# Kernel tuning notes

Hardware: AMD Instinct MI355X
Metric: run time of the kernel (lower is better)

The kernel has to match this reference:

```python
import jax, jax.numpy as jnp
import numpy as np

EPS = 1e-5
DEG = 2  # polynomial degree of each resgconv layer (adj powers 0..DEG-1)


def _bn(x):
    # repo's functional batchnorm(x, axis=1): standardize over the node axis per event
    m = x.mean(axis=1, keepdims=True)
    s = x.std(axis=1, keepdims=True)
    return (x - m) / (s + EPS)


def _adj(phi, eta):
    # Gaussian kernel of squared euclidean distance in the (eta, phi) plane
    d2 = (phi[:, :, None] - phi[:, None, :]) ** 2 + (eta[:, :, None] - eta[:, None, :]) ** 2
    return jnp.exp(-d2)  # [B, N, N]


def _resgconv(adj, x, W, b, Wr, br):
    # x: [B, C_in, N]; spread = concat of adj^k @ x for k in 0..DEG-1 over channels
    sp = [x]
    cur = x
    for _ in range(DEG - 1):
        cur = jnp.einsum('bij,bcj->bci', adj, cur)
        sp.append(cur)
    sp = jnp.concatenate(sp, axis=1)  # [B, C_in*DEG, N]
    out = jnp.einsum('oc,bcn->bon', W, sp) + b[None, :, None]
    res = jnp.einsum('oc,bcn->bon', Wr, x) + br[None, :, None]  # residual shortcut
    return jax.nn.relu(out) + res


def setup_inputs():
    key = jax.random.key(0)
    ks = jax.random.split(key, 32)
    B, N = 16, 2048
    dims = [3, 64, 64, 64, 64]
    inp = {
        'e': jax.random.normal(ks[0], (B, N), dtype=jnp.float32),
        'phi': jax.random.normal(ks[1], (B, N), dtype=jnp.float32),
        'eta': jax.random.normal(ks[2], (B, N), dtype=jnp.float32),
    }
    for i in range(4):
        cin, cout = dims[i], dims[i + 1]
        inp[f'W{i}'] = jax.random.normal(ks[3 + 4 * i], (cout, cin * DEG)) * (1.0 / np.sqrt(cin * DEG))
        inp[f'b{i}'] = jnp.zeros((cout,), dtype=jnp.float32)
        inp[f'Wr{i}'] = jax.random.normal(ks[4 + 4 * i], (cout, cin)) * (1.0 / np.sqrt(cin))
        inp[f'br{i}'] = jnp.zeros((cout,), dtype=jnp.float32)
    inp['fcW'] = jax.random.normal(ks[30], (1, dims[-1])) * (1.0 / np.sqrt(dims[-1]))
    inp['fcb'] = jnp.zeros((1,), dtype=jnp.float32)
    return inp


def reference(e, phi, eta, W0, b0, Wr0, br0, W1, b1, Wr1, br1, W2, b2, Wr2, br2, W3, b3, Wr3, br3, fcW, fcb):
    en = _bn(e)
    adj = _adj(phi, eta)
    x = jnp.stack([en, _bn(eta), _bn(phi)], axis=1)  # [B, 3, N]
    for (W, b, Wr, br) in ((W0, b0, Wr0, br0), (W1, b1, Wr1, br1), (W2, b2, Wr2, br2), (W3, b3, Wr3, br3)):
        x = _resgconv(adj, x, W, b, Wr, br)
    pooled = x.mean(axis=2)  # [B, C]
    out = pooled @ fcW.T + fcb  # [B, 1]
    return out[:, 0]
```

## Files before the change

### kernel.cpp

```cpp
#include <hip/hip_runtime.h>
#include <hip/hip_bf16.h>

#define NN 2048
#define NB 16
#define CAT_PITCH 136
#define XT_OFF 16384
#define SMEM_BYTES 81920

typedef __attribute__((ext_vector_type(8))) short short8;
typedef __attribute__((ext_vector_type(4))) float f32x4;

static __device__ __forceinline__ float bfbits2f(short s) {
  unsigned int u = ((unsigned int)(unsigned short)s) << 16;
  float f; __builtin_memcpy(&f, &u, 4); return f;
}
static __device__ __forceinline__ short f2bfbits(float f) {
  __hip_bfloat16 h = __float2bfloat16(f);
  unsigned short us; __builtin_memcpy(&us, &h, 2); return (short)us;
}
static __device__ __forceinline__ float exp2_fast(float x) {
#if __has_builtin(__builtin_amdgcn_exp2f)
  return __builtin_amdgcn_exp2f(x);
#else
  return exp2f(x);
#endif
}
static __device__ __forceinline__ unsigned pack2bf(float f0, float f1) {
  unsigned u0, u1;
  __builtin_memcpy(&u0, &f0, 4);
  __builtin_memcpy(&u1, &f1, 4);
  return __builtin_amdgcn_perm(u1 + 0x8000u, u0 + 0x8000u, 0x07060302u);
}
static __device__ __forceinline__ void gload_lds16(const void* g, void* l) {
  __builtin_amdgcn_global_load_lds(
      (const __attribute__((address_space(1))) unsigned int*)g,
      (__attribute__((address_space(3))) unsigned int*)l, 16, 0, 0);
}

__global__ __launch_bounds__(256) void bnprep_kernel(
    const float* __restrict__ e, const float* __restrict__ phi,
    const float* __restrict__ eta, __hip_bfloat16* __restrict__ x0,
    const float* __restrict__ W0, const float* __restrict__ W1,
    const float* __restrict__ W2, const float* __restrict__ W3,
    const float* __restrict__ R0, const float* __restrict__ R1,
    const float* __restrict__ R2, const float* __restrict__ R3,
    short* __restrict__ blob) {
  const int t = threadIdx.x;
  if (blockIdx.y == 64) {
    const int layer = blockIdx.x;
    if (layer >= 4) return;
    const float* W = layer == 0 ? W0 : layer == 1 ? W1 : layer == 2 ? W2 : W3;
    const float* R = layer == 0 ? R0 : layer == 1 ? R1 : layer == 2 ? R2 : R3;
    const int CIN = layer == 0 ? 3 : 64;
    short* base = blob + layer * 24576;
    for (int f = t; f < 8192; f += 256) {
      int e8 = f & 7, ln = (f >> 3) & 63, ks = (f >> 9) & 3, os = f >> 11;
      int o = os * 16 + (ln & 15);
      int k = ks * 32 + (ln >> 4) * 8 + e8;
      float v = 0.f;
      if (k < 64) { if (k < CIN) v = W[o * 2 * CIN + k]; }
      else { int c = k - 64; if (c < CIN) v = W[o * 2 * CIN + CIN + c]; }
      short hi = f2bfbits(v);
      base[f] = hi;
      base[8192 + f] = f2bfbits(v - bfbits2f(hi));
    }
    for (int f = t; f < 4096; f += 256) {
      int e8 = f & 7, ln = (f >> 3) & 63, ks = (f >> 9) & 1, os = f >> 10;
      int o = os * 16 + (ln & 15);
      int k = ks * 32 + (ln >> 4) * 8 + e8;
      float v = (k < CIN) ? R[o * CIN + k] : 0.f;
      short hi = f2bfbits(v);
      base[16384 + f] = hi;
      base[20480 + f] = f2bfbits(v - bfbits2f(hi));
    }
    return;
  }
  const int b = blockIdx.x;
  const int c = blockIdx.y;
  __hip_bfloat16* out = x0 + ((size_t)b * 64 + c) * NN;
  if (c >= 3) {
    short8 z = {0, 0, 0, 0, 0, 0, 0, 0};
    for (int idx = t * 8; idx < NN; idx += 256 * 8) *(short8*)&out[idx] = z;
    return;
  }
  const float* src = (c == 0 ? e : (c == 1 ? eta : phi)) + (size_t)b * NN;
  float sum = 0.f, sq = 0.f;
  for (int idx = t * 4; idx < NN; idx += 256 * 4) {
    float4 v = *(const float4*)&src[idx];
    sum += v.x + v.y + v.z + v.w;
    sq += v.x * v.x + v.y * v.y + v.z * v.z + v.w * v.w;
  }
  __shared__ float rs[256], rq[256];
  rs[t] = sum; rq[t] = sq;
  __syncthreads();
  for (int off = 128; off > 0; off >>= 1) {
    if (t < off) { rs[t] += rs[t + off]; rq[t] += rq[t + off]; }
    __syncthreads();
  }
  const float m = rs[0] * (1.f / NN);
  const float var = fmaxf(rq[0] * (1.f / NN) - m * m, 0.f);
  const float rinv = 1.f / (sqrtf(var) + 1e-5f);
  for (int idx = t * 4; idx < NN; idx += 256 * 4) {
    float4 v = *(const float4*)&src[idx];
    out[idx + 0] = __float2bfloat16((v.x - m) * rinv);
    out[idx + 1] = __float2bfloat16((v.y - m) * rinv);
    out[idx + 2] = __float2bfloat16((v.z - m) * rinv);
    out[idx + 3] = __float2bfloat16((v.w - m) * rinv);
  }
}

__global__ __launch_bounds__(512, 4) void layer_kernel(
    const float* __restrict__ phi, const float* __restrict__ eta,
    const __hip_bfloat16* __restrict__ x, const short* __restrict__ wcat,
    const short* __restrict__ wrb, const float* __restrict__ bias,
    const float* __restrict__ brs, __hip_bfloat16* __restrict__ xo) {
  const int bid = blockIdx.x;
  const int sid = (bid & 7) * 64 + (bid >> 3);
  const int b = sid >> 5;
  const int i0 = (sid & 31) * 64;
  const int tid = threadIdx.x;
  const int wave = tid >> 6;
  const int lane = tid & 63;
  const int c0 = lane & 15;
  const int hh = lane >> 4;
  const int koff = hh * 8;
  const int rh = wave & 1;
  const int jg = wave >> 1;

  __shared__ __align__(16) char smem[SMEM_BYTES];
  float* phs = (float*)smem;
  float* ehs = phs + NN;

  const float SC = 1.20112240872f;
  {
    const float* pb = phi + (size_t)b * NN;
    const float* eb = eta + (size_t)b * NN;
    for (int idx = tid; idx < NN; idx += 512) {
      phs[idx] = pb[idx] * SC;
      ehs[idx] = eb[idx] * SC;
    }
  }
  const short* xb = (const short*)(x + (size_t)b * 64 * NN);

  const int d4 = lane & 1, d5 = (lane >> 1) & 1, d6 = (lane >> 2) & 1;
  const int d7 = (lane >> 3) & 1, d8 = (lane >> 4) & 1, d9 = (lane >> 5) & 1;
  const int ch_l = (d9 << 3) | (d8 << 2) | (d7 << 1) | (d6 ^ d8);
  const int jb8 = ((d5 ^ d7) << 1) | (d4 ^ d6 ^ d8);
  char* wbuf = smem + XT_OFF + wave * 8192;

#define STAGE(tt)                                                             \
  {                                                                           \
    const int _t = (tt);                                                      \
    _Pragma("unroll")                                                         \
    for (int gsl = 0; gsl < 4; ++gsl)                                         \
      gload_lds16(xb + (size_t)(gsl * 16 + ch_l) * NN + jg * 512 + _t * 32 +  \
                      jb8 * 8,                                                \
                  wbuf + (_t & 1) * 4096 + gsl * 1024);                       \
  }

  STAGE(0);
  __syncthreads();

  float pi_[2], ei_[2];
#pragma unroll
  for (int mt = 0; mt < 2; ++mt) {
    const int row = i0 + rh * 32 + mt * 16 + c0;
    pi_[mt] = phs[row];
    ei_[mt] = ehs[row];
  }

  f32x4 acc[2][4];
#pragma unroll
  for (int mt = 0; mt < 2; ++mt)
#pragma unroll
    for (int cs = 0; cs < 4; ++cs) acc[mt][cs] = (f32x4){0.f, 0.f, 0.f, 0.f};

#define COMPUTE(tt)                                                           \
  {                                                                           \
    const int _t = (tt);                                                      \
    const char* xbuf = wbuf + (_t & 1) * 4096;                                \
    const int jb = jg * 512 + _t * 32 + koff;                                 \
    float pj[8], ej[8];                                                       \
    *(float4*)&pj[0] = *(const float4*)&phs[jb];                              \
    *(float4*)&pj[4] = *(const float4*)&phs[jb + 4];                          \
    *(float4*)&ej[0] = *(const float4*)&ehs[jb];                              \
    *(float4*)&ej[4] = *(const float4*)&ehs[jb + 4];                          \
    short8 af[2];                                                             \
    _Pragma("unroll")                                                         \
    for (int mt = 0; mt < 2; ++mt) {                                          \
      unsigned au[4];                                                         \
      _Pragma("unroll")                                                       \
      for (int pp = 0; pp < 4; ++pp) {                                        \
        float dpa = pi_[mt] - pj[2 * pp],     dea = ei_[mt] - ej[2 * pp];     \
        float dpb = pi_[mt] - pj[2 * pp + 1], deb = ei_[mt] - ej[2 * pp + 1]; \
        float fa = exp2_fast(-(dpa * dpa + dea * dea));                       \
        float fb = exp2_fast(-(dpb * dpb + deb * deb));                       \
        au[pp] = pack2bf(fa, fb);                                             \
      }                                                                       \
      __builtin_memcpy(&af[mt], au, 16);                                      \
    }                                                                         \
    _Pragma("unroll")                                                         \
    for (int cs = 0; cs < 4; ++cs) {                                          \
      short8 bf = *(const short8*)(xbuf + cs * 1024 +                         \
                                   ((c0 * 64 + koff * 2) ^ ((c0 & 7) << 4))); \
      _Pragma("unroll")                                                       \
      for (int mt = 0; mt < 2; ++mt)                                          \
        acc[mt][cs] = __builtin_amdgcn_mfma_f32_16x16x32_bf16(af[mt], bf,     \
                                                          acc[mt][cs], 0, 0, 0); \
    }                                                                         \
  }

#pragma unroll 1
  for (int t = 0; t < 15; ++t) {
    STAGE(t + 1);
    __builtin_amdgcn_sched_barrier(0);
    asm volatile("s_waitcnt vmcnt(4)" ::: "memory");
    __builtin_amdgcn_sched_barrier(0);
    COMPUTE(t);
    __builtin_amdgcn_sched_barrier(0);
  }
  asm volatile("s_waitcnt vmcnt(0)" ::: "memory");
  __builtin_amdgcn_sched_barrier(0);
  COMPUTE(15);
  __syncthreads();

  char* xt = smem + XT_OFF;
  if (jg >= 2) {
    float* sp = (float*)(xt + (rh * 2 + (jg - 2)) * 8192);
#pragma unroll
    for (int mt = 0; mt < 2; ++mt)
#pragma unroll
      for (int cs = 0; cs < 4; ++cs)
        *(f32x4*)&sp[((mt * 4 + cs) * 64 + lane) * 4] = acc[mt][cs];
  }
  __syncthreads();
  if (jg < 2) {
    const float* sp = (const float*)(xt + (rh * 2 + jg) * 8192);
#pragma unroll
    for (int mt = 0; mt < 2; ++mt)
#pragma unroll
      for (int cs = 0; cs < 4; ++cs)
        acc[mt][cs] += *(const f32x4*)&sp[((mt * 4 + cs) * 64 + lane) * 4];
  }
  __syncthreads();
  if (jg == 1) {
    float* sp = (float*)(xt + rh * 8192);
#pragma unroll
    for (int mt = 0; mt < 2; ++mt)
#pragma unroll
      for (int cs = 0; cs < 4; ++cs)
        *(f32x4*)&sp[((mt * 4 + cs) * 64 + lane) * 4] = acc[mt][cs];
  }
  __syncthreads();
  if (jg == 0) {
    const float* sp = (const float*)(xt + rh * 8192);
#pragma unroll
    for (int mt = 0; mt < 2; ++mt)
#pragma unroll
      for (int cs = 0; cs < 4; ++cs)
        acc[mt][cs] += *(const f32x4*)&sp[((mt * 4 + cs) * 64 + lane) * 4];
  }
  __syncthreads();

  short* cat = (short*)(smem + XT_OFF);
  short* out_t = (short*)(smem + XT_OFF + 64 * CAT_PITCH * 2);
  if (jg == 0) {
#pragma unroll
    for (int mt = 0; mt < 2; ++mt)
#pragma unroll
      for (int cs = 0; cs < 4; ++cs)
#pragma unroll
        for (int r = 0; r < 4; ++r) {
          const int irow = rh * 32 + mt * 16 + hh * 4 + r;
          cat[irow * CAT_PITCH + 64 + cs * 16 + c0] = f2bfbits(acc[mt][cs][r]);
        }
  }
  {
    const int cch = tid & 63, rp = tid >> 6;
    short8 v = *(const short8*)&xb[(size_t)cch * NN + i0 + rp * 8];
#pragma unroll
    for (int q = 0; q < 8; ++q) cat[(rp * 8 + q) * CAT_PITCH + cch] = v[q];
  }
  __syncthreads();

  {
    const int it = wave & 3;
    const int oh = wave >> 2;
    const int irl = it * 16 + c0;
    short8 bfx[4];
#pragma unroll
    for (int ks = 0; ks < 4; ++ks)
      bfx[ks] = *(const short8*)&cat[irl * CAT_PITCH + ks * 32 + koff];
#pragma unroll
    for (int osl = 0; osl < 2; ++osl) {
      const int os = oh * 2 + osl;
      f32x4 a1 = (f32x4){0.f, 0.f, 0.f, 0.f};
      f32x4 a2 = (f32x4){0.f, 0.f, 0.f, 0.f};
#pragma unroll
      for (int ks = 0; ks < 4; ++ks) {
        short8 whi = *(const short8*)&wcat[(size_t)(((os * 4 + ks) * 64) + lane) * 8];
        short8 wlo = *(const short8*)&wcat[8192 + (size_t)(((os * 4 + ks) * 64) + lane) * 8];
        a1 = __builtin_amdgcn_mfma_f32_16x16x32_bf16(whi, bfx[ks], a1, 0, 0, 0);
        a1 = __builtin_amdgcn_mfma_f32_16x16x32_bf16(wlo, bfx[ks], a1, 0, 0, 0);
      }
#pragma unroll
      for (int ks = 0; ks < 2; ++ks) {
        short8 rhi = *(const short8*)&wrb[(size_t)(((os * 2 + ks) * 64) + lane) * 8];
        short8 rlo = *(const short8*)&wrb[4096 + (size_t)(((os * 2 + ks) * 64) + lane) * 8];
        a2 = __builtin_amdgcn_mfma_f32_16x16x32_bf16(rhi, bfx[ks], a2, 0, 0, 0);
        a2 = __builtin_amdgcn_mfma_f32_16x16x32_bf16(rlo, bfx[ks], a2, 0, 0, 0);
      }
#pragma unroll
      for (int r = 0; r < 4; ++r) {
        const int o = os * 16 + hh * 4 + r;
        float v = fmaxf(a1[r] + bias[o], 0.f) + a2[r] + brs[o];
        out_t[o * CAT_PITCH + it * 16 + c0] = f2bfbits(v);
      }
    }
  }
  __syncthreads();

  {
    const int o = tid >> 3, part = tid & 7;
    short8 v = *(const short8*)&out_t[o * CAT_PITCH + part * 8];
    *(short8*)((short*)xo + (size_t)b * 64 * NN + (size_t)o * NN + i0 + part * 8) = v;
  }
#undef STAGE
#undef COMPUTE
}

__global__ __launch_bounds__(256) void final_kernel(
    const __hip_bfloat16* __restrict__ x, const float* __restrict__ fcW,
    const float* __restrict__ fcb, float* __restrict__ out) {
  const int b = blockIdx.x;
  const short* xb = (const short*)(x + (size_t)b * 64 * NN);
  float acc = 0.f;
  for (int f = threadIdx.x * 8; f < 64 * NN; f += 256 * 8) {
    short8 v = *(const short8*)&xb[f];
    const float w = fcW[f >> 11];
    float ss = 0.f;
#pragma unroll
    for (int e8 = 0; e8 < 8; ++e8) ss += bfbits2f(v[e8]);
    acc += w * ss;
  }
  __shared__ float red[256];
  red[threadIdx.x] = acc;
  __syncthreads();
  for (int off = 128; off > 0; off >>= 1) {
    if ((int)threadIdx.x < off) red[threadIdx.x] += red[threadIdx.x + off];
    __syncthreads();
  }
  if (threadIdx.x == 0) out[b] = red[0] * (1.f / NN) + fcb[0];
}

extern "C" void kernel_launch(void* const* d_in, const int* in_sizes, int n_in,
                              void* d_out, int out_size, void* d_ws, size_t ws_size,
                              hipStream_t stream) {
  const float* e   = (const float*)d_in[0];
  const float* phi = (const float*)d_in[1];
  const float* eta = (const float*)d_in[2];
  const float* W[4]  = {(const float*)d_in[3],  (const float*)d_in[7],
                        (const float*)d_in[11], (const float*)d_in[15]};
  const float* bb[4] = {(const float*)d_in[4],  (const float*)d_in[8],
                        (const float*)d_in[12], (const float*)d_in[16]};
  const float* Wr[4] = {(const float*)d_in[5],  (const float*)d_in[9],
                        (const float*)d_in[13], (const float*)d_in[17]};
  const float* br[4] = {(const float*)d_in[6],  (const float*)d_in[10],
                        (const float*)d_in[14], (const float*)d_in[18]};
  const float* fcW = (const float*)d_in[19];
  const float* fcb = (const float*)d_in[20];
  float* outp = (float*)d_out;

  const size_t XSZ = (size_t)NB * 64 * NN;
  __hip_bfloat16* xA = (__hip_bfloat16*)d_ws;
  __hip_bfloat16* xB = xA + XSZ;
  short* blob = (short*)(xB + XSZ);

  bnprep_kernel<<<dim3(16, 65), 256, 0, stream>>>(
      e, phi, eta, xA, W[0], W[1], W[2], W[3], Wr[0], Wr[1], Wr[2], Wr[3], blob);

  const __hip_bfloat16* xin = xA;
  __hip_bfloat16* xout = xB;
  for (int l = 0; l < 4; ++l) {
    const short* lb = blob + l * 24576;
    layer_kernel<<<512, 512, 0, stream>>>(phi, eta, xin, lb, lb + 16384,
                                          bb[l], br[l], xout);
    const __hip_bfloat16* t = xout; xout = (__hip_bfloat16*)xin; xin = t;
  }
  final_kernel<<<NB, 256, 0, stream>>>(xA, fcW, fcb, outp);
}
```

Baseline: 245.1 us.

## Precompute adjacency once in bf16 fragment layout and stream it into layer kernels

Adds an adj_kernel that computes the Gaussian adjacency for all events once, in bf16 and in the MFMA A-fragment order, and stores it in workspace. Each of the four layer kernels then loads those fragments from global memory instead of recomputing exp of squared distances, with a two-deep software pipeline for the adjacency and x loads. This removes repeated transcendental work at the cost of about 128 MB of adjacency traffic per layer read from HBM or cache, plus a larger working set.

Measured after the change: 272.7 us. +11.3%, slower.

```diff
diff --git a/kernel.cpp b/kernel.cpp
--- a/kernel.cpp
+++ b/kernel.cpp
@@ -4,8 +4,7 @@
 #define NN 2048
 #define NB 16
 #define CAT_PITCH 136
-#define XT_OFF 16384
-#define SMEM_BYTES 81920
+#define SMEM_BYTES 65536
 
 typedef __attribute__((ext_vector_type(8))) short short8;
 typedef __attribute__((ext_vector_type(4))) float f32x4;
@@ -109,11 +108,51 @@
   }
 }
 
+__global__ __launch_bounds__(256) void adj_kernel(
+    const float* __restrict__ phi, const float* __restrict__ eta,
+    short* __restrict__ adjT) {
+  const int bid = blockIdx.x;
+  const int b = bid >> 7;
+  const int it = bid & 127;
+  const int tid = threadIdx.x;
+  const int w = tid >> 6;
+  const int lane = tid & 63;
+  const int c0 = lane & 15;
+  const int hh = lane >> 4;
+  const float SC2 = 1.44269504089f;
+  const float* pb = phi + (size_t)b * NN;
+  const float* eb = eta + (size_t)b * NN;
+  const float pr = pb[it * 16 + c0];
+  const float er = eb[it * 16 + c0];
+  short* outb = adjT + ((size_t)b * 128 + it) * 64 * 512;
+#pragma unroll 2
+  for (int jt = w * 16; jt < w * 16 + 16; ++jt) {
+    const int j0 = jt * 32 + hh * 8;
+    float pj[8], ej[8];
+    *(float4*)&pj[0] = *(const float4*)&pb[j0];
+    *(float4*)&pj[4] = *(const float4*)&pb[j0 + 4];
+    *(float4*)&ej[0] = *(const float4*)&eb[j0];
+    *(float4*)&ej[4] = *(const float4*)&eb[j0 + 4];
+    unsigned au[4];
+#pragma unroll
+    for (int pp = 0; pp < 4; ++pp) {
+      float dpa = pr - pj[2 * pp],     dea = er - ej[2 * pp];
+      float dpb = pr - pj[2 * pp + 1], deb = er - ej[2 * pp + 1];
+      float d2a = dpa * dpa + dea * dea;
+      float d2b = dpb * dpb + deb * deb;
+      au[pp] = pack2bf(exp2_fast(-SC2 * d2a), exp2_fast(-SC2 * d2b));
+    }
+    short8 af;
+    __builtin_memcpy(&af, au, 16);
+    *(short8*)(outb + jt * 512 + lane * 8) = af;
+  }
+}
+
 __global__ __launch_bounds__(512, 4) void layer_kernel(
-    const float* __restrict__ phi, const float* __restrict__ eta,
-    const __hip_bfloat16* __restrict__ x, const short* __restrict__ wcat,
-    const short* __restrict__ wrb, const float* __restrict__ bias,
-    const float* __restrict__ brs, __hip_bfloat16* __restrict__ xo) {
+    const __hip_bfloat16* __restrict__ x, const short* __restrict__ adjT,
+    const short* __restrict__ wcat, const short* __restrict__ wrb,
+    const float* __restrict__ bias, const float* __restrict__ brs,
+    __hip_bfloat16* __restrict__ xo) {
   const int bid = blockIdx.x;
   const int sid = (bid & 7) * 64 + (bid >> 3);
   const int b = sid >> 5;
@@ -128,25 +167,16 @@
   const int jg = wave >> 1;
 
   __shared__ __align__(16) char smem[SMEM_BYTES];
-  float* phs = (float*)smem;
-  float* ehs = phs + NN;
-
-  const float SC = 1.20112240872f;
-  {
-    const float* pb = phi + (size_t)b * NN;
-    const float* eb = eta + (size_t)b * NN;
-    for (int idx = tid; idx < NN; idx += 512) {
-      phs[idx] = pb[idx] * SC;
-      ehs[idx] = eb[idx] * SC;
-    }
-  }
   const short* xb = (const short*)(x + (size_t)b * 64 * NN);
 
   const int d4 = lane & 1, d5 = (lane >> 1) & 1, d6 = (lane >> 2) & 1;
   const int d7 = (lane >> 3) & 1, d8 = (lane >> 4) & 1, d9 = (lane >> 5) & 1;
   const int ch_l = (d9 << 3) | (d8 << 2) | (d7 << 1) | (d6 ^ d8);
   const int jb8 = ((d5 ^ d7) << 1) | (d4 ^ d6 ^ d8);
-  char* wbuf = smem + XT_OFF + wave * 8192;
+  char* wbuf = smem + wave * 8192;
+
+  const short* atb = adjT +
+      (((size_t)b * 128 + (i0 >> 4) + rh * 2) * 64 + jg * 16) * 512 + lane * 8;
 
 #define STAGE(tt)                                                             \
   {                                                                           \
@@ -157,74 +187,56 @@
                       jb8 * 8,                                                \
                   wbuf + (_t & 1) * 4096 + gsl * 1024);                       \
   }
-
-  STAGE(0);
-  __syncthreads();
-
-  float pi_[2], ei_[2];
-#pragma unroll
-  for (int mt = 0; mt < 2; ++mt) {
-    const int row = i0 + rh * 32 + mt * 16 + c0;
-    pi_[mt] = phs[row];
-    ei_[mt] = ehs[row];
-  }
-
-  f32x4 acc[2][4];
-#pragma unroll
-  for (int mt = 0; mt < 2; ++mt)
-#pragma unroll
-    for (int cs = 0; cs < 4; ++cs) acc[mt][cs] = (f32x4){0.f, 0.f, 0.f, 0.f};
-
-#define COMPUTE(tt)                                                           \
+#define AFLOAD(tt, AF)                                                        \
   {                                                                           \
-    const int _t = (tt);                                                      \
-    const char* xbuf = wbuf + (_t & 1) * 4096;                                \
-    const int jb = jg * 512 + _t * 32 + koff;                                 \
-    float pj[8], ej[8];                                                       \
-    *(float4*)&pj[0] = *(const float4*)&phs[jb];                              \
-    *(float4*)&pj[4] = *(const float4*)&phs[jb + 4];                          \
-    *(float4*)&ej[0] = *(const float4*)&ehs[jb];                              \
-    *(float4*)&ej[4] = *(const float4*)&ehs[jb + 4];                          \
-    short8 af[2];                                                             \
-    _Pragma("unroll")                                                         \
-    for (int mt = 0; mt < 2; ++mt) {                                          \
-      unsigned au[4];                                                         \
-      _Pragma("unroll")                                                       \
-      for (int pp = 0; pp < 4; ++pp) {                                        \
-        float dpa = pi_[mt] - pj[2 * pp],     dea = ei_[mt] - ej[2 * pp];     \
-        float dpb = pi_[mt] - pj[2 * pp + 1], deb = ei_[mt] - ej[2 * pp + 1]; \
-        float fa = exp2_fast(-(dpa * dpa + dea * dea));                       \
-        float fb = exp2_fast(-(dpb * dpb + deb * deb));                       \
-        au[pp] = pack2bf(fa, fb);                                             \
-      }                                                                       \
-      __builtin_memcpy(&af[mt], au, 16);                                      \
-    }                                                                         \
+    AF##0 = *(const short8*)(atb + (tt) * 512);                               \
+    AF##1 = *(const short8*)(atb + 32768 + (tt) * 512);                       \
+  }
+#define COMPUTE(tt, AF)                                                       \
+  {                                                                           \
+    const char* xbuf = wbuf + ((tt) & 1) * 4096;                              \
     _Pragma("unroll")                                                         \
     for (int cs = 0; cs < 4; ++cs) {                                          \
       short8 bf = *(const short8*)(xbuf + cs * 1024 +                         \
                                    ((c0 * 64 + koff * 2) ^ ((c0 & 7) << 4))); \
-      _Pragma("unroll")                                                       \
-      for (int mt = 0; mt < 2; ++mt)                                          \
-        acc[mt][cs] = __builtin_amdgcn_mfma_f32_16x16x32_bf16(af[mt], bf,     \
-                                                          acc[mt][cs], 0, 0, 0); \
+      acc[0][cs] = __builtin_amdgcn_mfma_f32_16x16x32_bf16(AF##0, bf,         \
+                                                           acc[0][cs], 0, 0, 0); \
+      acc[1][cs] = __builtin_amdgcn_mfma_f32_16x16x32_bf16(AF##1, bf,         \
+                                                           acc[1][cs], 0, 0, 0); \
     }                                                                         \
   }
 
+  f32x4 acc[2][4];
+#pragma unroll
+  for (int mt = 0; mt < 2; ++mt)
+#pragma unroll
+    for (int cs = 0; cs < 4; ++cs) acc[mt][cs] = (f32x4){0.f, 0.f, 0.f, 0.f};
+
+  short8 afA0, afA1, afB0, afB1;
+  AFLOAD(0, afA) STAGE(0)
+  AFLOAD(1, afB) STAGE(1)
 #pragma unroll 1
-  for (int t = 0; t < 15; ++t) {
-    STAGE(t + 1);
+  for (int t = 0; t < 14; t += 2) {
+    asm volatile("s_waitcnt vmcnt(6)" ::: "memory");
     __builtin_amdgcn_sched_barrier(0);
-    asm volatile("s_waitcnt vmcnt(4)" ::: "memory");
+    COMPUTE(t, afA)
+    AFLOAD(t + 2, afA) STAGE(t + 2)
     __builtin_amdgcn_sched_barrier(0);
-    COMPUTE(t);
+    asm volatile("s_waitcnt vmcnt(6)" ::: "memory");
     __builtin_amdgcn_sched_barrier(0);
-  }
+    COMPUTE(t + 1, afB)
+    AFLOAD(t + 3, afB) STAGE(t + 3)
+    __builtin_amdgcn_sched_barrier(0);
+  }
+  asm volatile("s_waitcnt vmcnt(6)" ::: "memory");
+  __builtin_amdgcn_sched_barrier(0);
+  COMPUTE(14, afA)
   asm volatile("s_waitcnt vmcnt(0)" ::: "memory");
   __builtin_amdgcn_sched_barrier(0);
-  COMPUTE(15);
-  __syncthreads();
-
-  char* xt = smem + XT_OFF;
+  COMPUTE(15, afB)
+  __syncthreads();
+
+  char* xt = smem;
   if (jg >= 2) {
     float* sp = (float*)(xt + (rh * 2 + (jg - 2)) * 8192);
 #pragma unroll
@@ -262,8 +274,8 @@
   }
   __syncthreads();
 
-  short* cat = (short*)(smem + XT_OFF);
-  short* out_t = (short*)(smem + XT_OFF + 64 * CAT_PITCH * 2);
+  short* cat = (short*)smem;
+  short* out_t = (short*)(smem + 64 * CAT_PITCH * 2);
   if (jg == 0) {
 #pragma unroll
     for (int mt = 0; mt < 2; ++mt)
@@ -326,6 +338,7 @@
     *(short8*)((short*)xo + (size_t)b * 64 * NN + (size_t)o * NN + i0 + part * 8) = v;
   }
 #undef STAGE
+#undef AFLOAD
 #undef COMPUTE
 }
 
@@ -375,15 +388,17 @@
   __hip_bfloat16* xA = (__hip_bfloat16*)d_ws;
   __hip_bfloat16* xB = xA + XSZ;
   short* blob = (short*)(xB + XSZ);
+  short* adjT = (short*)((char*)d_ws + (16u << 20));
 
   bnprep_kernel<<<dim3(16, 65), 256, 0, stream>>>(
       e, phi, eta, xA, W[0], W[1], W[2], W[3], Wr[0], Wr[1], Wr[2], Wr[3], blob);
+  adj_kernel<<<NB * 128, 256, 0, stream>>>(phi, eta, adjT);
 
   const __hip_bfloat16* xin = xA;
   __hip_bfloat16* xout = xB;
   for (int l = 0; l < 4; ++l) {
     const short* lb = blob + l * 24576;
-    layer_kernel<<<512, 512, 0, stream>>>(phi, eta, xin, lb, lb + 16384,
+    layer_kernel<<<512, 512, 0, stream>>>(xin, adjT, lb, lb + 16384,
                                           bb[l], br[l], xout);
     const __hip_bfloat16* t = xout; xout = (__hip_bfloat16*)xin; xin = t;
   }
```

## Fuse four layer launches into one persistent kernel with per-batch grid barriers

Applied to the files above, without the earlier changes.

Replaces the four per-layer kernel launches with a single kernel that loops over the layers. Between layers, the 32 blocks sharing a batch element synchronise through an atomic counter in global memory. phi and eta are staged into LDS once and reused across all layers, and the block-to-batch mapping is changed so each batch's blocks are co-resident. This removes launch gaps and repeated prologue work, but it relies on all 512 blocks being resident at once. The spin-wait has a timeout that breaks out silently, which could produce wrong results if blocks are not co-scheduled.

Measured after the change: 306.9 us. 25.2% more time.

```diff
diff --git a/kernel.cpp b/kernel.cpp
--- a/kernel.cpp
+++ b/kernel.cpp
@@ -109,15 +109,19 @@
   }
 }
 
-__global__ __launch_bounds__(512, 4) void layer_kernel(
+__global__ __launch_bounds__(512, 4) void mega_kernel(
     const float* __restrict__ phi, const float* __restrict__ eta,
-    const __hip_bfloat16* __restrict__ x, const short* __restrict__ wcat,
-    const short* __restrict__ wrb, const float* __restrict__ bias,
-    const float* __restrict__ brs, __hip_bfloat16* __restrict__ xo) {
+    short* __restrict__ xA, short* __restrict__ xB,
+    const short* __restrict__ blob,
+    const float* __restrict__ B0, const float* __restrict__ B1,
+    const float* __restrict__ B2, const float* __restrict__ B3,
+    const float* __restrict__ Q0, const float* __restrict__ Q1,
+    const float* __restrict__ Q2, const float* __restrict__ Q3,
+    unsigned* __restrict__ bar) {
   const int bid = blockIdx.x;
-  const int sid = (bid & 7) * 64 + (bid >> 3);
-  const int b = sid >> 5;
-  const int i0 = (sid & 31) * 64;
+  const int q = bid >> 3;
+  const int b = (bid & 7) * 2 + (q >> 5);
+  const int i0 = (q & 31) * 64;
   const int tid = threadIdx.x;
   const int wave = tid >> 6;
   const int lane = tid & 63;
@@ -140,7 +144,15 @@
       ehs[idx] = eb[idx] * SC;
     }
   }
-  const short* xb = (const short*)(x + (size_t)b * 64 * NN);
+  __syncthreads();
+
+  float pi_[2], ei_[2];
+#pragma unroll
+  for (int mt = 0; mt < 2; ++mt) {
+    const int row = i0 + rh * 32 + mt * 16 + c0;
+    pi_[mt] = phs[row];
+    ei_[mt] = ehs[row];
+  }
 
   const int d4 = lane & 1, d5 = (lane >> 1) & 1, d6 = (lane >> 2) & 1;
   const int d7 = (lane >> 3) & 1, d8 = (lane >> 4) & 1, d9 = (lane >> 5) & 1;
@@ -153,28 +165,10 @@
     const int _t = (tt);                                                      \
     _Pragma("unroll")                                                         \
     for (int gsl = 0; gsl < 4; ++gsl)                                         \
-      gload_lds16(xb + (size_t)(gsl * 16 + ch_l) * NN + jg * 512 + _t * 32 +  \
+      gload_lds16(xbL + (size_t)(gsl * 16 + ch_l) * NN + jg * 512 + _t * 32 + \
                       jb8 * 8,                                                \
                   wbuf + (_t & 1) * 4096 + gsl * 1024);                       \
   }
-
-  STAGE(0);
-  __syncthreads();
-
-  float pi_[2], ei_[2];
-#pragma unroll
-  for (int mt = 0; mt < 2; ++mt) {
-    const int row = i0 + rh * 32 + mt * 16 + c0;
-    pi_[mt] = phs[row];
-    ei_[mt] = ehs[row];
-  }
-
-  f32x4 acc[2][4];
-#pragma unroll
-  for (int mt = 0; mt < 2; ++mt)
-#pragma unroll
-    for (int cs = 0; cs < 4; ++cs) acc[mt][cs] = (f32x4){0.f, 0.f, 0.f, 0.f};
-
 #define COMPUTE(tt)                                                           \
   {                                                                           \
     const int _t = (tt);                                                      \
@@ -211,119 +205,154 @@
   }
 
 #pragma unroll 1
-  for (int t = 0; t < 15; ++t) {
-    STAGE(t + 1);
+  for (int l = 0; l < 4; ++l) {
+    const short* xin = (l & 1) ? xB : xA;
+    short* xout = (l & 1) ? xA : xB;
+    const short* blobL = blob + l * 24576;
+    const short* wcat = blobL;
+    const short* wrb = blobL + 16384;
+    const float* bias = l == 0 ? B0 : l == 1 ? B1 : l == 2 ? B2 : B3;
+    const float* brs  = l == 0 ? Q0 : l == 1 ? Q1 : l == 2 ? Q2 : Q3;
+    const short* xbL = xin + (size_t)b * 64 * NN;
+
+    f32x4 acc[2][4];
+#pragma unroll
+    for (int mt = 0; mt < 2; ++mt)
+#pragma unroll
+      for (int cs = 0; cs < 4; ++cs) acc[mt][cs] = (f32x4){0.f, 0.f, 0.f, 0.f};
+
+    STAGE(0)
+#pragma unroll 1
+    for (int t = 0; t < 15; ++t) {
+      STAGE(t + 1);
+      __builtin_amdgcn_sched_barrier(0);
+      asm volatile("s_waitcnt vmcnt(4)" ::: "memory");
+      __builtin_amdgcn_sched_barrier(0);
+      COMPUTE(t);
+      __builtin_amdgcn_sched_barrier(0);
+    }
+    asm volatile("s_waitcnt vmcnt(0)" ::: "memory");
     __builtin_amdgcn_sched_barrier(0);
-    asm volatile("s_waitcnt vmcnt(4)" ::: "memory");
-    __builtin_amdgcn_sched_barrier(0);
-    COMPUTE(t);
-    __builtin_amdgcn_sched_barrier(0);
-  }
-  asm volatile("s_waitcnt vmcnt(0)" ::: "memory");
-  __builtin_amdgcn_sched_barrier(0);
-  COMPUTE(15);
-  __syncthreads();
-
-  char* xt = smem + XT_OFF;
-  if (jg >= 2) {
-    float* sp = (float*)(xt + (rh * 2 + (jg - 2)) * 8192);
-#pragma unroll
-    for (int mt = 0; mt < 2; ++mt)
-#pragma unroll
-      for (int cs = 0; cs < 4; ++cs)
-        *(f32x4*)&sp[((mt * 4 + cs) * 64 + lane) * 4] = acc[mt][cs];
-  }
-  __syncthreads();
-  if (jg < 2) {
-    const float* sp = (const float*)(xt + (rh * 2 + jg) * 8192);
-#pragma unroll
-    for (int mt = 0; mt < 2; ++mt)
-#pragma unroll
-      for (int cs = 0; cs < 4; ++cs)
-        acc[mt][cs] += *(const f32x4*)&sp[((mt * 4 + cs) * 64 + lane) * 4];
-  }
-  __syncthreads();
-  if (jg == 1) {
-    float* sp = (float*)(xt + rh * 8192);
-#pragma unroll
-    for (int mt = 0; mt < 2; ++mt)
-#pragma unroll
-      for (int cs = 0; cs < 4; ++cs)
-        *(f32x4*)&sp[((mt * 4 + cs) * 64 + lane) * 4] = acc[mt][cs];
-  }
-  __syncthreads();
-  if (jg == 0) {
-    const float* sp = (const float*)(xt + rh * 8192);
-#pragma unroll
-    for (int mt = 0; mt < 2; ++mt)
-#pragma unroll
-      for (int cs = 0; cs < 4; ++cs)
-        acc[mt][cs] += *(const f32x4*)&sp[((mt * 4 + cs) * 64 + lane) * 4];
-  }
-  __syncthreads();
-
-  short* cat = (short*)(smem + XT_OFF);
-  short* out_t = (short*)(smem + XT_OFF + 64 * CAT_PITCH * 2);
-  if (jg == 0) {
-#pragma unroll
-    for (int mt = 0; mt < 2; ++mt)
-#pragma unroll
-      for (int cs = 0; cs < 4; ++cs)
+    COMPUTE(15);
+    __syncthreads();
+
+    char* xt = smem + XT_OFF;
+    if (jg >= 2) {
+      float* sp = (float*)(xt + (rh * 2 + (jg - 2)) * 8192);
+#pragma unroll
+      for (int mt = 0; mt < 2; ++mt)
+#pragma unroll
+        for (int cs = 0; cs < 4; ++cs)
+          *(f32x4*)&sp[((mt * 4 + cs) * 64 + lane) * 4] = acc[mt][cs];
+    }
+    __syncthreads();
+    if (jg < 2) {
+      const float* sp = (const float*)(xt + (rh * 2 + jg) * 8192);
+#pragma unroll
+      for (int mt = 0; mt < 2; ++mt)
+#pragma unroll
+        for (int cs = 0; cs < 4; ++cs)
+          acc[mt][cs] += *(const f32x4*)&sp[((mt * 4 + cs) * 64 + lane) * 4];
+    }
+    __syncthreads();
+    if (jg == 1) {
+      float* sp = (float*)(xt + rh * 8192);
+#pragma unroll
+      for (int mt = 0; mt < 2; ++mt)
+#pragma unroll
+        for (int cs = 0; cs < 4; ++cs)
+          *(f32x4*)&sp[((mt * 4 + cs) * 64 + lane) * 4] = acc[mt][cs];
+    }
+    __syncthreads();
+    if (jg == 0) {
+      const float* sp = (const float*)(xt + rh * 8192);
+#pragma unroll
+      for (int mt = 0; mt < 2; ++mt)
+#pragma unroll
+        for (int cs = 0; cs < 4; ++cs)
+          acc[mt][cs] += *(const f32x4*)&sp[((mt * 4 + cs) * 64 + lane) * 4];
+    }
+    __syncthreads();
+
+    short* cat = (short*)(smem + XT_OFF);
+    short* out_t = (short*)(smem + XT_OFF + 64 * CAT_PITCH * 2);
+    if (jg == 0) {
+#pragma unroll
+      for (int mt = 0; mt < 2; ++mt)
+#pragma unroll
+        for (int cs = 0; cs < 4; ++cs)
+#pragma unroll
+          for (int r = 0; r < 4; ++r) {
+            const int irow = rh * 32 + mt * 16 + hh * 4 + r;
+            cat[irow * CAT_PITCH + 64 + cs * 16 + c0] = f2bfbits(acc[mt][cs][r]);
+          }
+    }
+    {
+      const int cch = tid & 63, rp = tid >> 6;
+      short8 v = *(const short8*)&xbL[(size_t)cch * NN + i0 + rp * 8];
+#pragma unroll
+      for (int qq = 0; qq < 8; ++qq) cat[(rp * 8 + qq) * CAT_PITCH + cch] = v[qq];
+    }
+    __syncthreads();
+
+    {
+      const int it = wave & 3;
+      const int oh = wave >> 2;
+      const int irl = it * 16 + c0;
+      short8 bfx[4];
+#pragma unroll
+      for (int ks = 0; ks < 4; ++ks)
+        bfx[ks] = *(const short8*)&cat[irl * CAT_PITCH + ks * 32 + koff];
+#pragma unroll
+      for (int osl = 0; osl < 2; ++osl) {
+        const int os = oh * 2 + osl;
+        f32x4 a1 = (f32x4){0.f, 0.f, 0.f, 0.f};
+        f32x4 a2 = (f32x4){0.f, 0.f, 0.f, 0.f};
+#pragma unroll
+        for (int ks = 0; ks < 4; ++ks) {
+          short8 whi = *(const short8*)&wcat[(size_t)(((os * 4 + ks) * 64) + lane) * 8];
+          short8 wlo = *(const short8*)&wcat[8192 + (size_t)(((os * 4 + ks) * 64) + lane) * 8];
+          a1 = __builtin_amdgcn_mfma_f32_16x16x32_bf16(whi, bfx[ks], a1, 0, 0, 0);
+          a1 = __builtin_amdgcn_mfma_f32_16x16x32_bf16(wlo, bfx[ks], a1, 0, 0, 0);
+        }
+#pragma unroll
+        for (int ks = 0; ks < 2; ++ks) {
+          short8 rhi = *(const short8*)&wrb[(size_t)(((os * 2 + ks) * 64) + lane) * 8];
+          short8 rlo = *(const short8*)&wrb[4096 + (size_t)(((os * 2 + ks) * 64) + lane) * 8];
+          a2 = __builtin_amdgcn_mfma_f32_16x16x32_bf16(rhi, bfx[ks], a2, 0, 0, 0);
+          a2 = __builtin_amdgcn_mfma_f32_16x16x32_bf16(rlo, bfx[ks], a2, 0, 0, 0);
+        }
 #pragma unroll
         for (int r = 0; r < 4; ++r) {
-          const int irow = rh * 32 + mt * 16 + hh * 4 + r;
-          cat[irow * CAT_PITCH + 64 + cs * 16 + c0] = f2bfbits(acc[mt][cs][r]);
+          const int o = os * 16 + hh * 4 + r;
+          float v = fmaxf(a1[r] + bias[o], 0.f) + a2[r] + brs[o];
+          out_t[o * CAT_PITCH + it * 16 + c0] = f2bfbits(v);
         }
-  }
-  {
-    const int cch = tid & 63, rp = tid >> 6;
-    short8 v = *(const short8*)&xb[(size_t)cch * NN + i0 + rp * 8];
-#pragma unroll
-    for (int q = 0; q < 8; ++q) cat[(rp * 8 + q) * CAT_PITCH + cch] = v[q];
-  }
-  __syncthreads();
-
-  {
-    const int it = wave & 3;
-    const int oh = wave >> 2;
-    const int irl = it * 16 + c0;
-    short8 bfx[4];
-#pragma unroll
-    for (int ks = 0; ks < 4; ++ks)
-      bfx[ks] = *(const short8*)&cat[irl * CAT_PITCH + ks * 32 + koff];
-#pragma unroll
-    for (int osl = 0; osl < 2; ++osl) {
-      const int os = oh * 2 + osl;
-      f32x4 a1 = (f32x4){0.f, 0.f, 0.f, 0.f};
-      f32x4 a2 = (f32x4){0.f, 0.f, 0.f, 0.f};
-#pragma unroll
-      for (int ks = 0; ks < 4; ++ks) {
-        short8 whi = *(const short8*)&wcat[(size_t)(((os * 4 + ks) * 64) + lane) * 8];
-        short8 wlo = *(const short8*)&wcat[8192 + (size_t)(((os * 4 + ks) * 64) + lane) * 8];
-        a1 = __builtin_amdgcn_mfma_f32_16x16x32_bf16(whi, bfx[ks], a1, 0, 0, 0);
-        a1 = __builtin_amdgcn_mfma_f32_16x16x32_bf16(wlo, bfx[ks], a1, 0, 0, 0);
       }
-#pragma unroll
-      for (int ks = 0; ks < 2; ++ks) {
-        short8 rhi = *(const short8*)&wrb[(size_t)(((os * 2 + ks) * 64) + lane) * 8];
-        short8 rlo = *(const short8*)&wrb[4096 + (size_t)(((os * 2 + ks) * 64) + lane) * 8];
-        a2 = __builtin_amdgcn_mfma_f32_16x16x32_bf16(rhi, bfx[ks], a2, 0, 0, 0);
-        a2 = __builtin_amdgcn_mfma_f32_16x16x32_bf16(rlo, bfx[ks], a2, 0, 0, 0);
+    }
+    __syncthreads();
+
+    {
+      const int o = tid >> 3, part = tid & 7;
+      short8 v = *(const short8*)&out_t[o * CAT_PITCH + part * 8];
+      *(short8*)(xout + (size_t)b * 64 * NN + (size_t)o * NN + i0 + part * 8) = v;
+    }
+
+    if (l < 3) {
+      __syncthreads();
+      if (tid == 0) {
+        unsigned* slot = &bar[b * 4 + l];
+        __hip_atomic_fetch_add(slot, 1u, __ATOMIC_RELEASE, __HIP_MEMORY_SCOPE_AGENT);
+        long cnt = 0;
+        while (__hip_atomic_load(slot, __ATOMIC_RELAXED, __HIP_MEMORY_SCOPE_AGENT) < 32u) {
+          __builtin_amdgcn_s_sleep(4);
+          if (++cnt > (1L << 21)) break;
+        }
+        (void)__hip_atomic_load(slot, __ATOMIC_ACQUIRE, __HIP_MEMORY_SCOPE_AGENT);
       }
-#pragma unroll
-      for (int r = 0; r < 4; ++r) {
-        const int o = os * 16 + hh * 4 + r;
-        float v = fmaxf(a1[r] + bias[o], 0.f) + a2[r] + brs[o];
-        out_t[o * CAT_PITCH + it * 16 + c0] = f2bfbits(v);
-      }
-    }
-  }
-  __syncthreads();
-
-  {
-    const int o = tid >> 3, part = tid & 7;
-    short8 v = *(const short8*)&out_t[o * CAT_PITCH + part * 8];
-    *(short8*)((short*)xo + (size_t)b * 64 * NN + (size_t)o * NN + i0 + part * 8) = v;
+      __syncthreads();
+      asm volatile("" ::: "memory");
+    }
   }
 #undef STAGE
 #undef COMPUTE
@@ -375,17 +404,15 @@
   __hip_bfloat16* xA = (__hip_bfloat16*)d_ws;
   __hip_bfloat16* xB = xA + XSZ;
   short* blob = (short*)(xB + XSZ);
-
+  unsigned* bar = (unsigned*)((char*)d_ws + (8u << 20) + (256u << 10));
+
+  hipMemsetAsync(bar, 0, 256, stream);
   bnprep_kernel<<<dim3(16, 65), 256, 0, stream>>>(
       e, phi, eta, xA, W[0], W[1], W[2], W[3], Wr[0], Wr[1], Wr[2], Wr[3], blob);
 
-  const __hip_bfloat16* xin = xA;
-  __hip_bfloat16* xout = xB;
-  for (int l = 0; l < 4; ++l) {
-    const short* lb = blob + l * 24576;
-    layer_kernel<<<512, 512, 0, stream>>>(phi, eta, xin, lb, lb + 16384,
-                                          bb[l], br[l], xout);
-    const __hip_bfloat16* t = xout; xout = (__hip_bfloat16*)xin; xin = t;
-  }
+  mega_kernel<<<512, 512, 0, stream>>>(
+      phi, eta, (short*)xA, (short*)xB, blob,
+      bb[0], bb[1], bb[2], bb[3], br[0], br[1], br[2], br[3], bar);
+
   final_kernel<<<NB, 256, 0, stream>>>(xA, fcW, fcb, outp);
 }
```
